# Kernel optimization log

Measured on AMD Instinct MI355X. Metric: run time of the kernel, lower is better.

Reference implementation:

```python
import jax, jax.numpy as jnp
import numpy as np

B, T, D, H = 8, 1024, 1024, 16
DK = D // H

def setup_inputs() -> dict:
    key = jax.random.key(0)
    ks = jax.random.split(key, 12)
    s = 0.02
    return {
        'query': jax.random.normal(ks[0], (B, T, D), jnp.float32),
        'key':   jax.random.normal(ks[1], (B, T, D), jnp.float32),
        'value': jax.random.normal(ks[2], (B, T, D), jnp.float32),
        'mask':  jnp.ones((B, T, T), dtype=bool),
        'Wq': jax.random.normal(ks[3], (D, D), jnp.float32) * s,
        'bq': jnp.zeros((D,), jnp.float32),
        'Wk': jax.random.normal(ks[4], (D, D), jnp.float32) * s,
        'bk': jnp.zeros((D,), jnp.float32),
        'Wv': jax.random.normal(ks[5], (D, D), jnp.float32) * s,
        'bv': jnp.zeros((D,), jnp.float32),
        'Wo': jax.random.normal(ks[6], (D, D), jnp.float32) * s,
        'bo': jnp.zeros((D,), jnp.float32),
    }

def reference(query, key, value, mask, Wq, bq, Wk, bk, Wv, bv, Wo, bo):
    # q,k,v: [B,H,T,DK] after projection + head split (torch Linear: x @ W.T + b)
    def proj(x, W, b):
        y = x @ W.T + b
        return y.reshape(B, -1, H, DK).transpose(0, 2, 1, 3)
    q = proj(query, Wq, bq)
    k = proj(key, Wk, bk)
    v = proj(value, Wv, bv)
    # cache is empty (size 0) in this config; new_cache = concat(k, v) on last dim
    new_cache = jnp.concatenate((k, v), axis=-1)  # [B,H,T,2*DK]
    scores = jnp.einsum('bhqd,bhkd->bhqk', q, k) / jnp.sqrt(jnp.float32(DK))
    # mask: [B,T,T] -> [B,1,T,T]; True = keep (masked_fill on eq(0))
    pad = (mask[:, None, :, :] == 0)
    scores = jnp.where(pad, -jnp.inf, scores)
    attn = jax.nn.softmax(scores, axis=-1)
    attn = jnp.where(pad, 0.0, attn)
    x = jnp.einsum('bhqk,bhkd->bhqd', attn, v)  # [B,H,T,DK]
    x = x.transpose(0, 2, 1, 3).reshape(B, -1, D)
    out = x @ Wo.T + bo
    return (out, new_cache)
```

## Files before the change

### kernel.cpp

```cpp
#include <hip/hip_runtime.h>
#include <hip/hip_bf16.h>
#include <stdint.h>


typedef __attribute__((ext_vector_type(8))) short short8;
typedef __attribute__((ext_vector_type(4))) short short4v;
typedef __attribute__((ext_vector_type(4))) float floatx4;

__device__ __forceinline__ void gld_lds16(const void* g, void* lds) {
  __builtin_amdgcn_global_load_lds(
      (const __attribute__((address_space(1))) uint32_t*)(uintptr_t)g,
      (__attribute__((address_space(3))) uint32_t*)(uintptr_t)lds, 16, 0, 0);
}

__device__ __forceinline__ short f2bf(float f) {
  uint32_t u = __builtin_bit_cast(uint32_t, f);
  u += 0x7fffu + ((u >> 16) & 1u);
  return (short)(u >> 16);
}

__global__ __launch_bounds__(256) void cvt_f32_bf16(
    const float* __restrict__ src, unsigned short* __restrict__ dst, int n8) {
  int i = blockIdx.x * 256 + threadIdx.x;
  if (i < n8) {
    const floatx4* p = (const floatx4*)(src + (size_t)i * 8);
    floatx4 a = p[0], b = p[1];
    short8 o;
    o[0] = f2bf(a[0]); o[1] = f2bf(a[1]); o[2] = f2bf(a[2]); o[3] = f2bf(a[3]);
    o[4] = f2bf(b[0]); o[5] = f2bf(b[1]); o[6] = f2bf(b[2]); o[7] = f2bf(b[3]);
    *(short8*)(dst + (size_t)i * 8) = o;
  }
}

__global__ __launch_bounds__(256) void gemm_bf16(
    const unsigned short* __restrict__ A,
    const unsigned short* __restrict__ W,
    const float* __restrict__ bias,
    float* __restrict__ outF,
    unsigned short* __restrict__ outB,
    int mode)
{
  __shared__ __align__(16) short As[128 * 32];
  __shared__ __align__(16) short Bs[128 * 32];
  const int tid = threadIdx.x;
  const int w = tid >> 6, L = tid & 63, quad = L >> 4, l15 = L & 15;
  const int m0 = blockIdx.x * 128, n0 = blockIdx.y * 128;
  const int mw = (w >> 1) * 64, nw = (w & 1) * 64;
  floatx4 acc[4][4] = {};

  for (int k0 = 0; k0 < 1024; k0 += 32) {
#pragma unroll
    for (int i = 0; i < 2; ++i) {
      int s = i * 256 + tid;
      int row = s >> 2, g = s & 3;
      gld_lds16(A + (size_t)(m0 + row) * 1024 + k0 + g * 8, &As[(i * 256 + w * 64) * 8]);
      gld_lds16(W + (size_t)(n0 + row) * 1024 + k0 + g * 8, &Bs[(i * 256 + w * 64) * 8]);
    }
    __syncthreads();
    short8 af[4], bf[4];
#pragma unroll
    for (int mt = 0; mt < 4; ++mt) {
      int row = mw + mt * 16 + l15;
      af[mt] = *(const short8*)&As[row * 32 + quad * 8];
    }
#pragma unroll
    for (int nt = 0; nt < 4; ++nt) {
      int row = nw + nt * 16 + l15;
      bf[nt] = *(const short8*)&Bs[row * 32 + quad * 8];
    }
#pragma unroll
    for (int mt = 0; mt < 4; ++mt)
#pragma unroll
      for (int nt = 0; nt < 4; ++nt)
        acc[mt][nt] = __builtin_amdgcn_mfma_f32_16x16x32_bf16(af[mt], bf[nt], acc[mt][nt], 0, 0, 0);
    __syncthreads();
  }

#pragma unroll
  for (int nt = 0; nt < 4; ++nt) {
    int col = n0 + nw + nt * 16 + l15;
    float bv = bias[col];
#pragma unroll
    for (int mt = 0; mt < 4; ++mt) {
      int rbase = m0 + mw + mt * 16 + quad * 4;
#pragma unroll
      for (int r = 0; r < 4; ++r) {
        int row = rbase + r;
        float v = acc[mt][nt][r] + bv;
        if (mode == 0) {
          outB[(size_t)row * 1024 + col] = (unsigned short)f2bf(v);
        } else if (mode == 3) {
          outF[(size_t)row * 1024 + col] = v;
        } else {
          int b = row >> 10, t = row & 1023;
          int h = col >> 6, dk = col & 63;
          size_t cbase = ((size_t)(b * 16 + h) * 1024 + t) * 128 + dk;
          if (mode == 1) {
            outF[cbase] = v;
          } else {
            outF[cbase + 64] = v;
            outB[((size_t)(b * 16 + h) * 64 + dk) * 1024 + t] = (unsigned short)f2bf(v);
          }
        }
      }
    }
  }
}

__global__ __launch_bounds__(256) void gemm_bt(
    const float* __restrict__ Af,
    const unsigned short* __restrict__ Ab,
    const float* __restrict__ W,
    const float* __restrict__ bias,
    float* __restrict__ outF,
    unsigned short* __restrict__ outB,
    int mode)
{
  __shared__ __align__(16) short As[128 * 32];
  __shared__ __align__(16) short Bs[128 * 32];
  const int tid = threadIdx.x;
  const int w = tid >> 6, L = tid & 63, quad = L >> 4, l15 = L & 15;
  const int m0 = blockIdx.x * 128, n0 = blockIdx.y * 128;
  const int mw = (w >> 1) * 64, nw = (w & 1) * 64;
  floatx4 acc[4][4] = {};

  for (int k0 = 0; k0 < 1024; k0 += 32) {
    if (mode == 3) {
#pragma unroll
      for (int i = 0; i < 2; ++i) {
        int s = i * 256 + tid;
        int row = s >> 2, g = s & 3;
        gld_lds16(Ab + (size_t)(m0 + row) * 1024 + k0 + g * 8, &As[(i * 256 + w * 64) * 8]);
      }
    } else {
#pragma unroll
      for (int i = 0; i < 2; ++i) {
        int s = i * 256 + tid;
        int row = s >> 2, g = s & 3;
        const float* p = Af + (size_t)(m0 + row) * 1024 + k0 + g * 8;
        floatx4 x0 = *(const floatx4*)p;
        floatx4 x1 = *(const floatx4*)(p + 4);
        short8 cv;
        cv[0] = f2bf(x0[0]); cv[1] = f2bf(x0[1]); cv[2] = f2bf(x0[2]); cv[3] = f2bf(x0[3]);
        cv[4] = f2bf(x1[0]); cv[5] = f2bf(x1[1]); cv[6] = f2bf(x1[2]); cv[7] = f2bf(x1[3]);
        *(short8*)&As[s * 8] = cv;
      }
    }
#pragma unroll
    for (int i = 0; i < 2; ++i) {
      int s = i * 256 + tid;
      int row = s >> 2, g = s & 3;
      const float* p = W + (size_t)(n0 + row) * 1024 + k0 + g * 8;
      floatx4 x0 = *(const floatx4*)p;
      floatx4 x1 = *(const floatx4*)(p + 4);
      short8 cv;
      cv[0] = f2bf(x0[0]); cv[1] = f2bf(x0[1]); cv[2] = f2bf(x0[2]); cv[3] = f2bf(x0[3]);
      cv[4] = f2bf(x1[0]); cv[5] = f2bf(x1[1]); cv[6] = f2bf(x1[2]); cv[7] = f2bf(x1[3]);
      *(short8*)&Bs[s * 8] = cv;
    }
    __syncthreads();
    short8 af[4], bf[4];
#pragma unroll
    for (int mt = 0; mt < 4; ++mt) {
      int row = mw + mt * 16 + l15;
      af[mt] = *(const short8*)&As[row * 32 + quad * 8];
    }
#pragma unroll
    for (int nt = 0; nt < 4; ++nt) {
      int row = nw + nt * 16 + l15;
      bf[nt] = *(const short8*)&Bs[row * 32 + quad * 8];
    }
#pragma unroll
    for (int mt = 0; mt < 4; ++mt)
#pragma unroll
      for (int nt = 0; nt < 4; ++nt)
        acc[mt][nt] = __builtin_amdgcn_mfma_f32_16x16x32_bf16(af[mt], bf[nt], acc[mt][nt], 0, 0, 0);
    __syncthreads();
  }

#pragma unroll
  for (int nt = 0; nt < 4; ++nt) {
    int col = n0 + nw + nt * 16 + l15;
    float bv = bias[col];
#pragma unroll
    for (int mt = 0; mt < 4; ++mt) {
      int rbase = m0 + mw + mt * 16 + quad * 4;
#pragma unroll
      for (int r = 0; r < 4; ++r) {
        int row = rbase + r;
        float v = acc[mt][nt][r] + bv;
        if (mode == 0) {
          outB[(size_t)row * 1024 + col] = (unsigned short)f2bf(v);
        } else if (mode == 3) {
          outF[(size_t)row * 1024 + col] = v;
        } else {
          int b = row >> 10, t = row & 1023;
          int h = col >> 6, dk = col & 63;
          size_t cbase = ((size_t)(b * 16 + h) * 1024 + t) * 128 + dk;
          if (mode == 1) {
            outF[cbase] = v;
          } else {
            outF[cbase + 64] = v;
            outB[((size_t)(b * 16 + h) * 64 + dk) * 1024 + t] = (unsigned short)f2bf(v);
          }
        }
      }
    }
  }
}

__global__ __launch_bounds__(256) void attn_kernel(
    const unsigned short* __restrict__ qws,
    const float* __restrict__ cacheF,
    const unsigned short* __restrict__ vt,
    unsigned short* __restrict__ xws)
{
  __shared__ __align__(16) short Ks[128 * 64];
  __shared__ __align__(16) short Vs[64 * 128];
  __shared__ __align__(16) short Ps[128 * 136];
  const int tid = threadIdx.x;
  const int w = tid >> 6, L = tid & 63, quad = L >> 4, l15 = L & 15;
  const int qt0 = blockIdx.x, bh = blockIdx.y;
  const int b = bh >> 4, h = bh & 15;
  const float Cs = 0.125f * 1.44269504088896340736f;

#pragma unroll
  for (int i = 0; i < 4; ++i) {
    int s = i * 256 + tid;
    int row = s >> 3, g = s & 7;
    gld_lds16(qws + (size_t)(b * 1024 + qt0 * 128 + row) * 1024 + h * 64 + g * 8,
              &Ps[(i * 256 + w * 64) * 8]);
  }
  __syncthreads();
  short8 qf[2][2];
#pragma unroll
  for (int qt = 0; qt < 2; ++qt) {
    int row = w * 32 + qt * 16 + l15;
#pragma unroll
    for (int hf = 0; hf < 2; ++hf)
      qf[qt][hf] = *(const short8*)&Ps[row * 64 + hf * 32 + quad * 8];
  }
  __syncthreads();

  float mrun[2] = {-1.0e30f, -1.0e30f};
  float lrun[2] = {0.f, 0.f};
  floatx4 oacc[2][4] = {};

  for (int tb = 0; tb < 8; ++tb) {
    int t0 = tb * 128;
#pragma unroll
    for (int i = 0; i < 4; ++i) {
      int s = i * 256 + tid;
      int row = s >> 4, j = (s & 15) ^ (row & 15);
      gld_lds16(vt + ((size_t)bh * 64 + row) * 1024 + t0 + j * 8,
                &Vs[(i * 256 + w * 64) * 8]);
    }
#pragma unroll
    for (int p = 0; p < 8; ++p) {
      int e = p * 256 + tid;
      int t = e >> 4, c4 = e & 15;
      const float* src = cacheF + ((size_t)bh * 1024 + t0 + t) * 128 + c4 * 4;
      floatx4 f = *(const floatx4*)src;
      short4v cv;
      cv[0] = f2bf(f[0]); cv[1] = f2bf(f[1]); cv[2] = f2bf(f[2]); cv[3] = f2bf(f[3]);
      int sl = ((c4 >> 1) ^ (t & 7));
      *(short4v*)&Ks[t * 64 + sl * 8 + (c4 & 1) * 4] = cv;
    }
    __syncthreads();

    floatx4 st[8][2];
#pragma unroll
    for (int kt = 0; kt < 8; ++kt) {
      int row = kt * 16 + l15;
      short8 a0 = *(const short8*)&Ks[row * 64 + (quad ^ (row & 7)) * 8];
      short8 a1 = *(const short8*)&Ks[row * 64 + ((quad | 4) ^ (row & 7)) * 8];
#pragma unroll
      for (int qt = 0; qt < 2; ++qt) {
        floatx4 c = {};
        c = __builtin_amdgcn_mfma_f32_16x16x32_bf16(a0, qf[qt][0], c, 0, 0, 0);
        c = __builtin_amdgcn_mfma_f32_16x16x32_bf16(a1, qf[qt][1], c, 0, 0, 0);
        st[kt][qt] = c;
      }
    }

    float alpha_s[2];
#pragma unroll
    for (int qt = 0; qt < 2; ++qt) {
      float tmax = -1.0e30f;
#pragma unroll
      for (int kt = 0; kt < 8; ++kt)
#pragma unroll
        for (int r = 0; r < 4; ++r) tmax = fmaxf(tmax, st[kt][qt][r]);
      tmax = fmaxf(tmax, __shfl_xor(tmax, 16));
      tmax = fmaxf(tmax, __shfl_xor(tmax, 32));
      float mnew = fmaxf(mrun[qt], tmax * Cs);
      alpha_s[qt] = exp2f(fminf(mrun[qt] - mnew, 0.f));
      mrun[qt] = mnew;
      float psum = 0.f;
      int q = w * 32 + qt * 16 + l15;
#pragma unroll
      for (int kt = 0; kt < 8; ++kt) {
        short4v pk;
#pragma unroll
        for (int r = 0; r < 4; ++r) {
          float p = exp2f(fminf(fmaf(st[kt][qt][r], Cs, -mnew), 0.f));
          psum += p;
          pk[r] = f2bf(p);
        }
        *(short4v*)&Ps[q * 136 + kt * 16 + quad * 4] = pk;
      }
      psum += __shfl_xor(psum, 16);
      psum += __shfl_xor(psum, 32);
      lrun[qt] = lrun[qt] * alpha_s[qt] + psum;
    }

#pragma unroll
    for (int mt = 0; mt < 2; ++mt)
#pragma unroll
      for (int r = 0; r < 4; ++r) {
        float a = __shfl(alpha_s[mt], quad * 4 + r);
#pragma unroll
        for (int nt = 0; nt < 4; ++nt) oacc[mt][nt][r] *= a;
      }

#pragma unroll
    for (int ks = 0; ks < 4; ++ks) {
      short8 pa[2], vb[4];
#pragma unroll
      for (int mt = 0; mt < 2; ++mt) {
        int q = w * 32 + mt * 16 + l15;
        pa[mt] = *(const short8*)&Ps[q * 136 + ks * 32 + quad * 8];
      }
#pragma unroll
      for (int nt = 0; nt < 4; ++nt) {
        int d = nt * 16 + l15;
        int sl = (ks * 4 + quad) ^ (d & 15);
        vb[nt] = *(const short8*)&Vs[d * 128 + sl * 8];
      }
#pragma unroll
      for (int mt = 0; mt < 2; ++mt)
#pragma unroll
        for (int nt = 0; nt < 4; ++nt)
          oacc[mt][nt] = __builtin_amdgcn_mfma_f32_16x16x32_bf16(pa[mt], vb[nt], oacc[mt][nt], 0, 0, 0);
    }
    __syncthreads();
  }

#pragma unroll
  for (int mt = 0; mt < 2; ++mt) {
    float linv0 = 1.0f / lrun[mt];
#pragma unroll
    for (int r = 0; r < 4; ++r) {
      float linv = __shfl(linv0, quad * 4 + r);
      int q = qt0 * 128 + w * 32 + mt * 16 + quad * 4 + r;
      size_t rowbase = ((size_t)(b * 1024 + q)) * 1024 + h * 64;
#pragma unroll
      for (int nt = 0; nt < 4; ++nt) {
        int d = nt * 16 + l15;
        xws[rowbase + d] = (unsigned short)f2bf(oacc[mt][nt][r] * linv);
      }
    }
  }
}

extern "C" void kernel_launch(void* const* d_in, const int* in_sizes, int n_in,
                              void* d_out, int out_size, void* d_ws, size_t ws_size,
                              hipStream_t stream) {
  (void)in_sizes; (void)n_in; (void)out_size;
  const float* query = (const float*)d_in[0];
  const float* key_  = (const float*)d_in[1];
  const float* value = (const float*)d_in[2];
  const float* Wq = (const float*)d_in[4];
  const float* bq = (const float*)d_in[5];
  const float* Wk = (const float*)d_in[6];
  const float* bk = (const float*)d_in[7];
  const float* Wv = (const float*)d_in[8];
  const float* bv = (const float*)d_in[9];
  const float* Wo = (const float*)d_in[10];
  const float* bo = (const float*)d_in[11];

  float* out   = (float*)d_out;
  float* cache = out + (size_t)8192 * 1024;
  unsigned short* ws = (unsigned short*)d_ws;
  const size_t MEG = 1u << 20;

  dim3 blk(256), gg(64, 8);
  if (ws_size >= (size_t)72 * MEG) {
    unsigned short* qin = ws;
    unsigned short* kin = ws + 8 * MEG;
    unsigned short* vin = ws + 16 * MEG;
    unsigned short* wq  = ws + 24 * MEG;
    unsigned short* wk  = ws + 25 * MEG;
    unsigned short* wv  = ws + 26 * MEG;
    unsigned short* wo  = ws + 27 * MEG;
    unsigned short* qbf = ws + 28 * MEG;
    unsigned short* vtw = qin;
    unsigned short* xbf = kin;

    cvt_f32_bf16<<<4096, blk, 0, stream>>>(query, qin, 1 << 20);
    cvt_f32_bf16<<<4096, blk, 0, stream>>>(key_,  kin, 1 << 20);
    cvt_f32_bf16<<<4096, blk, 0, stream>>>(value, vin, 1 << 20);
    cvt_f32_bf16<<<512,  blk, 0, stream>>>(Wq, wq, 1 << 17);
    cvt_f32_bf16<<<512,  blk, 0, stream>>>(Wk, wk, 1 << 17);
    cvt_f32_bf16<<<512,  blk, 0, stream>>>(Wv, wv, 1 << 17);
    cvt_f32_bf16<<<512,  blk, 0, stream>>>(Wo, wo, 1 << 17);

    gemm_bf16<<<gg, blk, 0, stream>>>(qin, wq, bq, nullptr, qbf, 0);
    gemm_bf16<<<gg, blk, 0, stream>>>(kin, wk, bk, cache, nullptr, 1);
    gemm_bf16<<<gg, blk, 0, stream>>>(vin, wv, bv, cache, vtw, 2);
    attn_kernel<<<dim3(8, 128), blk, 0, stream>>>(qbf, cache, vtw, xbf);
    gemm_bf16<<<gg, blk, 0, stream>>>(xbf, wo, bo, out, nullptr, 3);
  } else {
    unsigned short* qbf = ws;
    unsigned short* xbf = ws + 8 * MEG;
    unsigned short* vtw = ws + 16 * MEG;
    gemm_bt<<<gg, blk, 0, stream>>>(query, nullptr, Wq, bq, nullptr, qbf, 0);
    gemm_bt<<<gg, blk, 0, stream>>>(key_,  nullptr, Wk, bk, cache, nullptr, 1);
    gemm_bt<<<gg, blk, 0, stream>>>(value, nullptr, Wv, bv, cache, vtw, 2);
    attn_kernel<<<dim3(8, 128), blk, 0, stream>>>(qbf, cache, vtw, xbf);
    gemm_bt<<<gg, blk, 0, stream>>>(nullptr, xbf, Wo, bo, out, nullptr, 3);
  }
}
```

Baseline: 464.0 us.

## Emit bf16 K from projection, merge converts, share LDS, add setprio in attention

```diff
diff --git a/kernel.cpp b/kernel.cpp
--- a/kernel.cpp
+++ b/kernel.cpp
@@ -1,5 +1,4 @@
 #include <hip/hip_runtime.h>
-#include <hip/hip_bf16.h>
 #include <stdint.h>
 
 
@@ -19,16 +18,33 @@
   return (short)(u >> 16);
 }
 
-__global__ __launch_bounds__(256) void cvt_f32_bf16(
-    const float* __restrict__ src, unsigned short* __restrict__ dst, int n8) {
+__device__ __forceinline__ uint32_t cvtpk_bf16(float lo, float hi) {
+  uint32_t r;
+  asm("v_cvt_pk_bf16_f32 %0, %1, %2" : "=v"(r) : "v"(lo), "v"(hi));
+  return r;
+}
+
+__global__ __launch_bounds__(256) void cvt_multi(
+    const float* __restrict__ s0, unsigned short* __restrict__ d0,
+    const float* __restrict__ s1, unsigned short* __restrict__ d1,
+    const float* __restrict__ s2, unsigned short* __restrict__ d2,
+    const float* __restrict__ s3, unsigned short* __restrict__ d3,
+    int n8) {
+  const float* s;
+  unsigned short* d;
+  int y = blockIdx.y;
+  if (y == 0) { s = s0; d = d0; }
+  else if (y == 1) { s = s1; d = d1; }
+  else if (y == 2) { s = s2; d = d2; }
+  else { s = s3; d = d3; }
   int i = blockIdx.x * 256 + threadIdx.x;
   if (i < n8) {
-    const floatx4* p = (const floatx4*)(src + (size_t)i * 8);
+    const floatx4* p = (const floatx4*)(s + (size_t)i * 8);
     floatx4 a = p[0], b = p[1];
     short8 o;
     o[0] = f2bf(a[0]); o[1] = f2bf(a[1]); o[2] = f2bf(a[2]); o[3] = f2bf(a[3]);
     o[4] = f2bf(b[0]); o[5] = f2bf(b[1]); o[6] = f2bf(b[2]); o[7] = f2bf(b[3]);
-    *(short8*)(dst + (size_t)i * 8) = o;
+    *(short8*)(d + (size_t)i * 8) = o;
   }
 }
 
@@ -55,6 +71,109 @@
       int row = s >> 2, g = s & 3;
       gld_lds16(A + (size_t)(m0 + row) * 1024 + k0 + g * 8, &As[(i * 256 + w * 64) * 8]);
       gld_lds16(W + (size_t)(n0 + row) * 1024 + k0 + g * 8, &Bs[(i * 256 + w * 64) * 8]);
+    }
+    __syncthreads();
+    short8 af[4], bf[4];
+#pragma unroll
+    for (int mt = 0; mt < 4; ++mt) {
+      int row = mw + mt * 16 + l15;
+      af[mt] = *(const short8*)&As[row * 32 + quad * 8];
+    }
+#pragma unroll
+    for (int nt = 0; nt < 4; ++nt) {
+      int row = nw + nt * 16 + l15;
+      bf[nt] = *(const short8*)&Bs[row * 32 + quad * 8];
+    }
+#pragma unroll
+    for (int mt = 0; mt < 4; ++mt)
+#pragma unroll
+      for (int nt = 0; nt < 4; ++nt)
+        acc[mt][nt] = __builtin_amdgcn_mfma_f32_16x16x32_bf16(af[mt], bf[nt], acc[mt][nt], 0, 0, 0);
+    __syncthreads();
+  }
+
+#pragma unroll
+  for (int nt = 0; nt < 4; ++nt) {
+    int col = n0 + nw + nt * 16 + l15;
+    float bv = bias[col];
+#pragma unroll
+    for (int mt = 0; mt < 4; ++mt) {
+      int rbase = m0 + mw + mt * 16 + quad * 4;
+#pragma unroll
+      for (int r = 0; r < 4; ++r) {
+        int row = rbase + r;
+        float v = acc[mt][nt][r] + bv;
+        if (mode == 0) {
+          outB[(size_t)row * 1024 + col] = (unsigned short)f2bf(v);
+        } else if (mode == 3) {
+          outF[(size_t)row * 1024 + col] = v;
+        } else {
+          int b = row >> 10, t = row & 1023;
+          int h = col >> 6, dk = col & 63;
+          size_t cbase = ((size_t)(b * 16 + h) * 1024 + t) * 128 + dk;
+          if (mode == 1) {
+            outF[cbase] = v;
+            outB[((size_t)(b * 16 + h) * 1024 + t) * 64 + dk] = (unsigned short)f2bf(v);
+          } else {
+            outF[cbase + 64] = v;
+            outB[((size_t)(b * 16 + h) * 64 + dk) * 1024 + t] = (unsigned short)f2bf(v);
+          }
+        }
+      }
+    }
+  }
+}
+
+__global__ __launch_bounds__(256) void gemm_bt(
+    const float* __restrict__ Af,
+    const unsigned short* __restrict__ Ab,
+    const float* __restrict__ W,
+    const float* __restrict__ bias,
+    float* __restrict__ outF,
+    unsigned short* __restrict__ outB,
+    int mode)
+{
+  __shared__ __align__(16) short As[128 * 32];
+  __shared__ __align__(16) short Bs[128 * 32];
+  const int tid = threadIdx.x;
+  const int w = tid >> 6, L = tid & 63, quad = L >> 4, l15 = L & 15;
+  const int m0 = blockIdx.x * 128, n0 = blockIdx.y * 128;
+  const int mw = (w >> 1) * 64, nw = (w & 1) * 64;
+  floatx4 acc[4][4] = {};
+
+  for (int k0 = 0; k0 < 1024; k0 += 32) {
+    if (mode == 3) {
+#pragma unroll
+      for (int i = 0; i < 2; ++i) {
+        int s = i * 256 + tid;
+        int row = s >> 2, g = s & 3;
+        gld_lds16(Ab + (size_t)(m0 + row) * 1024 + k0 + g * 8, &As[(i * 256 + w * 64) * 8]);
+      }
+    } else {
+#pragma unroll
+      for (int i = 0; i < 2; ++i) {
+        int s = i * 256 + tid;
+        int row = s >> 2, g = s & 3;
+        const float* p = Af + (size_t)(m0 + row) * 1024 + k0 + g * 8;
+        floatx4 x0 = *(const floatx4*)p;
+        floatx4 x1 = *(const floatx4*)(p + 4);
+        short8 cv;
+        cv[0] = f2bf(x0[0]); cv[1] = f2bf(x0[1]); cv[2] = f2bf(x0[2]); cv[3] = f2bf(x0[3]);
+        cv[4] = f2bf(x1[0]); cv[5] = f2bf(x1[1]); cv[6] = f2bf(x1[2]); cv[7] = f2bf(x1[3]);
+        *(short8*)&As[s * 8] = cv;
+      }
+    }
+#pragma unroll
+    for (int i = 0; i < 2; ++i) {
+      int s = i * 256 + tid;
+      int row = s >> 2, g = s & 3;
+      const float* p = W + (size_t)(n0 + row) * 1024 + k0 + g * 8;
+      floatx4 x0 = *(const floatx4*)p;
+      floatx4 x1 = *(const floatx4*)(p + 4);
+      short8 cv;
+      cv[0] = f2bf(x0[0]); cv[1] = f2bf(x0[1]); cv[2] = f2bf(x0[2]); cv[3] = f2bf(x0[3]);
+      cv[4] = f2bf(x1[0]); cv[5] = f2bf(x1[1]); cv[6] = f2bf(x1[2]); cv[7] = f2bf(x1[3]);
+      *(short8*)&Bs[s * 8] = cv;
     }
     __syncthreads();
     short8 af[4], bf[4];
@@ -107,120 +226,18 @@
   }
 }
 
-__global__ __launch_bounds__(256) void gemm_bt(
-    const float* __restrict__ Af,
-    const unsigned short* __restrict__ Ab,
-    const float* __restrict__ W,
-    const float* __restrict__ bias,
-    float* __restrict__ outF,
-    unsigned short* __restrict__ outB,
-    int mode)
-{
-  __shared__ __align__(16) short As[128 * 32];
-  __shared__ __align__(16) short Bs[128 * 32];
-  const int tid = threadIdx.x;
-  const int w = tid >> 6, L = tid & 63, quad = L >> 4, l15 = L & 15;
-  const int m0 = blockIdx.x * 128, n0 = blockIdx.y * 128;
-  const int mw = (w >> 1) * 64, nw = (w & 1) * 64;
-  floatx4 acc[4][4] = {};
-
-  for (int k0 = 0; k0 < 1024; k0 += 32) {
-    if (mode == 3) {
-#pragma unroll
-      for (int i = 0; i < 2; ++i) {
-        int s = i * 256 + tid;
-        int row = s >> 2, g = s & 3;
-        gld_lds16(Ab + (size_t)(m0 + row) * 1024 + k0 + g * 8, &As[(i * 256 + w * 64) * 8]);
-      }
-    } else {
-#pragma unroll
-      for (int i = 0; i < 2; ++i) {
-        int s = i * 256 + tid;
-        int row = s >> 2, g = s & 3;
-        const float* p = Af + (size_t)(m0 + row) * 1024 + k0 + g * 8;
-        floatx4 x0 = *(const floatx4*)p;
-        floatx4 x1 = *(const floatx4*)(p + 4);
-        short8 cv;
-        cv[0] = f2bf(x0[0]); cv[1] = f2bf(x0[1]); cv[2] = f2bf(x0[2]); cv[3] = f2bf(x0[3]);
-        cv[4] = f2bf(x1[0]); cv[5] = f2bf(x1[1]); cv[6] = f2bf(x1[2]); cv[7] = f2bf(x1[3]);
-        *(short8*)&As[s * 8] = cv;
-      }
-    }
-#pragma unroll
-    for (int i = 0; i < 2; ++i) {
-      int s = i * 256 + tid;
-      int row = s >> 2, g = s & 3;
-      const float* p = W + (size_t)(n0 + row) * 1024 + k0 + g * 8;
-      floatx4 x0 = *(const floatx4*)p;
-      floatx4 x1 = *(const floatx4*)(p + 4);
-      short8 cv;
-      cv[0] = f2bf(x0[0]); cv[1] = f2bf(x0[1]); cv[2] = f2bf(x0[2]); cv[3] = f2bf(x0[3]);
-      cv[4] = f2bf(x1[0]); cv[5] = f2bf(x1[1]); cv[6] = f2bf(x1[2]); cv[7] = f2bf(x1[3]);
-      *(short8*)&Bs[s * 8] = cv;
-    }
-    __syncthreads();
-    short8 af[4], bf[4];
-#pragma unroll
-    for (int mt = 0; mt < 4; ++mt) {
-      int row = mw + mt * 16 + l15;
-      af[mt] = *(const short8*)&As[row * 32 + quad * 8];
-    }
-#pragma unroll
-    for (int nt = 0; nt < 4; ++nt) {
-      int row = nw + nt * 16 + l15;
-      bf[nt] = *(const short8*)&Bs[row * 32 + quad * 8];
-    }
-#pragma unroll
-    for (int mt = 0; mt < 4; ++mt)
-#pragma unroll
-      for (int nt = 0; nt < 4; ++nt)
-        acc[mt][nt] = __builtin_amdgcn_mfma_f32_16x16x32_bf16(af[mt], bf[nt], acc[mt][nt], 0, 0, 0);
-    __syncthreads();
-  }
-
-#pragma unroll
-  for (int nt = 0; nt < 4; ++nt) {
-    int col = n0 + nw + nt * 16 + l15;
-    float bv = bias[col];
-#pragma unroll
-    for (int mt = 0; mt < 4; ++mt) {
-      int rbase = m0 + mw + mt * 16 + quad * 4;
-#pragma unroll
-      for (int r = 0; r < 4; ++r) {
-        int row = rbase + r;
-        float v = acc[mt][nt][r] + bv;
-        if (mode == 0) {
-          outB[(size_t)row * 1024 + col] = (unsigned short)f2bf(v);
-        } else if (mode == 3) {
-          outF[(size_t)row * 1024 + col] = v;
-        } else {
-          int b = row >> 10, t = row & 1023;
-          int h = col >> 6, dk = col & 63;
-          size_t cbase = ((size_t)(b * 16 + h) * 1024 + t) * 128 + dk;
-          if (mode == 1) {
-            outF[cbase] = v;
-          } else {
-            outF[cbase + 64] = v;
-            outB[((size_t)(b * 16 + h) * 64 + dk) * 1024 + t] = (unsigned short)f2bf(v);
-          }
-        }
-      }
-    }
-  }
-}
-
 __global__ __launch_bounds__(256) void attn_kernel(
     const unsigned short* __restrict__ qws,
     const float* __restrict__ cacheF,
     const unsigned short* __restrict__ vt,
+    const unsigned short* __restrict__ kbf,
     unsigned short* __restrict__ xws)
 {
-  __shared__ __align__(16) short Ks[128 * 64];
+  __shared__ __align__(16) short Us[128 * 136];
   __shared__ __align__(16) short Vs[64 * 128];
-  __shared__ __align__(16) short Ps[128 * 136];
   const int tid = threadIdx.x;
   const int w = tid >> 6, L = tid & 63, quad = L >> 4, l15 = L & 15;
-  const int qt0 = blockIdx.x, bh = blockIdx.y;
+  const int bh = blockIdx.x, qt0 = blockIdx.y;
   const int b = bh >> 4, h = bh & 15;
   const float Cs = 0.125f * 1.44269504088896340736f;
 
@@ -229,7 +246,7 @@
     int s = i * 256 + tid;
     int row = s >> 3, g = s & 7;
     gld_lds16(qws + (size_t)(b * 1024 + qt0 * 128 + row) * 1024 + h * 64 + g * 8,
-              &Ps[(i * 256 + w * 64) * 8]);
+              &Us[(i * 256 + w * 64) * 8]);
   }
   __syncthreads();
   short8 qf[2][2];
@@ -238,7 +255,7 @@
     int row = w * 32 + qt * 16 + l15;
 #pragma unroll
     for (int hf = 0; hf < 2; ++hf)
-      qf[qt][hf] = *(const short8*)&Ps[row * 64 + hf * 32 + quad * 8];
+      qf[qt][hf] = *(const short8*)&Us[row * 64 + hf * 32 + quad * 8];
   }
   __syncthreads();
 
@@ -255,25 +272,36 @@
       gld_lds16(vt + ((size_t)bh * 64 + row) * 1024 + t0 + j * 8,
                 &Vs[(i * 256 + w * 64) * 8]);
     }
-#pragma unroll
-    for (int p = 0; p < 8; ++p) {
-      int e = p * 256 + tid;
-      int t = e >> 4, c4 = e & 15;
-      const float* src = cacheF + ((size_t)bh * 1024 + t0 + t) * 128 + c4 * 4;
-      floatx4 f = *(const floatx4*)src;
-      short4v cv;
-      cv[0] = f2bf(f[0]); cv[1] = f2bf(f[1]); cv[2] = f2bf(f[2]); cv[3] = f2bf(f[3]);
-      int sl = ((c4 >> 1) ^ (t & 7));
-      *(short4v*)&Ks[t * 64 + sl * 8 + (c4 & 1) * 4] = cv;
+    if (kbf) {
+#pragma unroll
+      for (int i = 0; i < 4; ++i) {
+        int s = i * 256 + tid;
+        int t = s >> 3, j = (s & 7) ^ (t & 7);
+        gld_lds16(kbf + ((size_t)bh * 1024 + t0 + t) * 64 + j * 8,
+                  &Us[(i * 256 + w * 64) * 8]);
+      }
+    } else {
+#pragma unroll
+      for (int p = 0; p < 8; ++p) {
+        int e = p * 256 + tid;
+        int t = e >> 4, c4 = e & 15;
+        const float* src = cacheF + ((size_t)bh * 1024 + t0 + t) * 128 + c4 * 4;
+        floatx4 f = *(const floatx4*)src;
+        short4v cv;
+        cv[0] = f2bf(f[0]); cv[1] = f2bf(f[1]); cv[2] = f2bf(f[2]); cv[3] = f2bf(f[3]);
+        int sl = ((c4 >> 1) ^ (t & 7));
+        *(short4v*)&Us[t * 64 + sl * 8 + (c4 & 1) * 4] = cv;
+      }
     }
     __syncthreads();
 
     floatx4 st[8][2];
+    __builtin_amdgcn_s_setprio(1);
 #pragma unroll
     for (int kt = 0; kt < 8; ++kt) {
       int row = kt * 16 + l15;
-      short8 a0 = *(const short8*)&Ks[row * 64 + (quad ^ (row & 7)) * 8];
-      short8 a1 = *(const short8*)&Ks[row * 64 + ((quad | 4) ^ (row & 7)) * 8];
+      short8 a0 = *(const short8*)&Us[row * 64 + (quad ^ (row & 7)) * 8];
+      short8 a1 = *(const short8*)&Us[row * 64 + ((quad | 4) ^ (row & 7)) * 8];
 #pragma unroll
       for (int qt = 0; qt < 2; ++qt) {
         floatx4 c = {};
@@ -282,6 +310,8 @@
         st[kt][qt] = c;
       }
     }
+    __builtin_amdgcn_s_setprio(0);
+    __syncthreads();
 
     float alpha_s[2];
 #pragma unroll
@@ -300,14 +330,15 @@
       int q = w * 32 + qt * 16 + l15;
 #pragma unroll
       for (int kt = 0; kt < 8; ++kt) {
-        short4v pk;
-#pragma unroll
-        for (int r = 0; r < 4; ++r) {
-          float p = exp2f(fminf(fmaf(st[kt][qt][r], Cs, -mnew), 0.f));
-          psum += p;
-          pk[r] = f2bf(p);
-        }
-        *(short4v*)&Ps[q * 136 + kt * 16 + quad * 4] = pk;
+        float p0 = exp2f(fminf(fmaf(st[kt][qt][0], Cs, -mnew), 0.f));
+        float p1 = exp2f(fminf(fmaf(st[kt][qt][1], Cs, -mnew), 0.f));
+        float p2 = exp2f(fminf(fmaf(st[kt][qt][2], Cs, -mnew), 0.f));
+        float p3 = exp2f(fminf(fmaf(st[kt][qt][3], Cs, -mnew), 0.f));
+        psum += (p0 + p1) + (p2 + p3);
+        uint32_t lo = cvtpk_bf16(p0, p1);
+        uint32_t hi = cvtpk_bf16(p2, p3);
+        *(uint64_t*)&Us[q * 136 + kt * 16 + quad * 4] =
+            (uint64_t)lo | ((uint64_t)hi << 32);
       }
       psum += __shfl_xor(psum, 16);
       psum += __shfl_xor(psum, 32);
@@ -323,13 +354,14 @@
         for (int nt = 0; nt < 4; ++nt) oacc[mt][nt][r] *= a;
       }
 
+    __builtin_amdgcn_s_setprio(1);
 #pragma unroll
     for (int ks = 0; ks < 4; ++ks) {
       short8 pa[2], vb[4];
 #pragma unroll
       for (int mt = 0; mt < 2; ++mt) {
         int q = w * 32 + mt * 16 + l15;
-        pa[mt] = *(const short8*)&Ps[q * 136 + ks * 32 + quad * 8];
+        pa[mt] = *(const short8*)&Us[q * 136 + ks * 32 + quad * 8];
       }
 #pragma unroll
       for (int nt = 0; nt < 4; ++nt) {
@@ -343,6 +375,7 @@
         for (int nt = 0; nt < 4; ++nt)
           oacc[mt][nt] = __builtin_amdgcn_mfma_f32_16x16x32_bf16(pa[mt], vb[nt], oacc[mt][nt], 0, 0, 0);
     }
+    __builtin_amdgcn_s_setprio(0);
     __syncthreads();
   }
 
@@ -395,20 +428,18 @@
     unsigned short* wo  = ws + 27 * MEG;
     unsigned short* qbf = ws + 28 * MEG;
     unsigned short* vtw = qin;
+    unsigned short* kbf = vin;
     unsigned short* xbf = kin;
 
-    cvt_f32_bf16<<<4096, blk, 0, stream>>>(query, qin, 1 << 20);
-    cvt_f32_bf16<<<4096, blk, 0, stream>>>(key_,  kin, 1 << 20);
-    cvt_f32_bf16<<<4096, blk, 0, stream>>>(value, vin, 1 << 20);
-    cvt_f32_bf16<<<512,  blk, 0, stream>>>(Wq, wq, 1 << 17);
-    cvt_f32_bf16<<<512,  blk, 0, stream>>>(Wk, wk, 1 << 17);
-    cvt_f32_bf16<<<512,  blk, 0, stream>>>(Wv, wv, 1 << 17);
-    cvt_f32_bf16<<<512,  blk, 0, stream>>>(Wo, wo, 1 << 17);
+    cvt_multi<<<dim3(4096, 3), blk, 0, stream>>>(
+        query, qin, key_, kin, value, vin, nullptr, nullptr, 1 << 20);
+    cvt_multi<<<dim3(512, 4), blk, 0, stream>>>(
+        Wq, wq, Wk, wk, Wv, wv, Wo, wo, 1 << 17);
 
     gemm_bf16<<<gg, blk, 0, stream>>>(qin, wq, bq, nullptr, qbf, 0);
-    gemm_bf16<<<gg, blk, 0, stream>>>(kin, wk, bk, cache, nullptr, 1);
     gemm_bf16<<<gg, blk, 0, stream>>>(vin, wv, bv, cache, vtw, 2);
-    attn_kernel<<<dim3(8, 128), blk, 0, stream>>>(qbf, cache, vtw, xbf);
+    gemm_bf16<<<gg, blk, 0, stream>>>(kin, wk, bk, cache, kbf, 1);
+    attn_kernel<<<dim3(128, 8), blk, 0, stream>>>(qbf, cache, vtw, kbf, xbf);
     gemm_bf16<<<gg, blk, 0, stream>>>(xbf, wo, bo, out, nullptr, 3);
   } else {
     unsigned short* qbf = ws;
@@ -417,7 +448,7 @@
     gemm_bt<<<gg, blk, 0, stream>>>(query, nullptr, Wq, bq, nullptr, qbf, 0);
     gemm_bt<<<gg, blk, 0, stream>>>(key_,  nullptr, Wk, bk, cache, nullptr, 1);
     gemm_bt<<<gg, blk, 0, stream>>>(value, nullptr, Wv, bv, cache, vtw, 2);
-    attn_kernel<<<dim3(8, 128), blk, 0, stream>>>(qbf, cache, vtw, xbf);
+    attn_kernel<<<dim3(128, 8), blk, 0, stream>>>(qbf, cache, vtw, nullptr, xbf);
     gemm_bt<<<gg, blk, 0, stream>>>(nullptr, xbf, Wo, bo, out, nullptr, 3);
   }
 }
```

After: 427.1 us. 8.0% less time.
